# Optimization experiments

Hardware: AMD Instinct MI355X
Metric: run time of the kernel (lower is better)

The kernel has to match this reference:

```python
import jax, jax.numpy as jnp
import numpy as np

WINDOW = 10
STRIDES = 1
EPS = 1e-5


def setup_inputs() -> dict:
    key = jax.random.key(0)
    B, T, F = 128, 512, 40
    tensors = jax.random.normal(key, (B, T, F), dtype=jnp.float32)
    return {"tensors": tensors}


def reference(tensors):
    # tensors: [B, T, F]
    B, T, F = tensors.shape
    # window start positions, replicating the module's iter_list logic
    starts = np.arange(0, T - WINDOW + 1, STRIDES)
    if (T - WINDOW) not in starts:
        starts = np.append(starts, T - WINDOW)
    # [S, W] gather indices -> windowed view [B, S, W, F]
    idx = starts[:, None] + np.arange(WINDOW)[None, :]
    xw = tensors[:, idx, :]  # [B, S, W, F]

    mean = xw.mean(axis=2)  # [B, S, F] == K.mean over window axis
    # K.std: population std (ddof=0) over the window axis
    std = jnp.sqrt(((xw - mean[:, :, None, :]) ** 2).mean(axis=2))  # [B, S, F]
    # K.switch(is_nan(std), mean-mean, std): NaN std -> 0
    std = jnp.where(jnp.isnan(std), jnp.zeros_like(std), std) + EPS

    # E[x_i * x_j] over window for all feature pairs: [B, S, F, F]
    Exy = jnp.einsum('bswi,bswj->bsij', xw, xw) / WINDOW
    cov = Exy - mean[:, :, :, None] * mean[:, :, None, :]
    corr = cov / (std[:, :, :, None] * std[:, :, None, :])  # [B, S, F, F]

    # itertools.combinations(range(F), 2) order == upper-triangular row-major
    iu, ju = np.triu_indices(F, 1)
    return corr[:, :, iu, ju]  # [B, S, C] with C = F*(F-1)/2
```

## Files before the change

kernel.cpp:

```cpp
#include <hip/hip_runtime.h>

#define BB   128
#define TT   512
#define FF   40
#define WW   10
#define NS   503
#define NP   780
#define SC   64
#define NCHUNK 8
#define ROWS (SC + WW - 1)
#define EPSC 1e-5f
#define C01  0.31622776601683794f

__global__ __launch_bounds__(256, 4) void ts_corr_r6(const float* __restrict__ in,
                                                     float* __restrict__ out) {
    const int blk = blockIdx.x;
    const int b   = blk / NCHUNK;
    const int c   = blk - b * NCHUNK;
    const int s0  = (c == NCHUNK - 1) ? (NS - SC) : c * SC;
    const int tid = threadIdx.x;

    __shared__ float  xs[SC + WW][FF];
    __shared__ float2 st[SC][FF];

    const float4* src4 = (const float4*)(in + ((size_t)b * TT + s0) * FF);
    float4* xs4 = (float4*)&xs[0][0];
    #pragma unroll
    for (int k = 0; k < 3; ++k) {
        const int i = tid + k * 256;
        if (i < ROWS * FF / 4) xs4[i] = src4[i];
    }
    __syncthreads();

    #pragma unroll
    for (int k = 0; k < 3; ++k) {
        const int qd = tid + k * 256;
        if (qd < SC * FF / 4) {
            const int t  = qd / 10;
            const int f0 = (qd - t * 10) * 4;
            float sx0=0,sx1=0,sx2=0,sx3=0, sq0=0,sq1=0,sq2=0,sq3=0;
            #pragma unroll
            for (int w = 0; w < WW; ++w) {
                const float4 x = *(const float4*)&xs[t + w][f0];
                sx0 += x.x; sx1 += x.y; sx2 += x.z; sx3 += x.w;
                sq0 += x.x*x.x; sq1 += x.y*x.y; sq2 += x.z*x.z; sq3 += x.w*x.w;
            }
            const float m0 = sx0*0.1f, m1 = sx1*0.1f, m2 = sx2*0.1f, m3 = sx3*0.1f;
            const float u0 = 1.f/(sqrtf(fmaxf(sq0*0.1f - m0*m0, 0.f)) + EPSC);
            const float u1 = 1.f/(sqrtf(fmaxf(sq1*0.1f - m1*m1, 0.f)) + EPSC);
            const float u2 = 1.f/(sqrtf(fmaxf(sq2*0.1f - m2*m2, 0.f)) + EPSC);
            const float u3 = 1.f/(sqrtf(fmaxf(sq3*0.1f - m3*m3, 0.f)) + EPSC);
            *(float4*)&st[t][f0]     = make_float4(u0*C01, m0*u0, u1*C01, m1*u1);
            *(float4*)&st[t][f0 + 2] = make_float4(u2*C01, m2*u2, u3*C01, m3*u3);
        }
    }

    int pi[4], pj[4];
    float sxy[4], ph[4][WW];
    #pragma unroll
    for (int k = 0; k < 4; ++k) {
        const int p = tid + k * 256;
        const int pp = (p < NP) ? p : 0;
        int i = (int)((79.0f - sqrtf((float)(6241 - 8 * pp))) * 0.5f);
        while (i > 0 && i * (79 - i) / 2 > pp) --i;
        while ((i + 1) * (79 - (i + 1)) / 2 <= pp) ++i;
        pi[k] = i;
        pj[k] = pp - i * (79 - i) / 2 + i + 1;
        float s = 0.f;
        #pragma unroll
        for (int w = 0; w < WW; ++w) {
            const float pr = xs[w][pi[k]] * xs[w][pj[k]];
            ph[k][w] = pr;
            s += pr;
        }
        sxy[k] = s;
    }
    __syncthreads();

    float* dst0 = out + (size_t)(b * NS + s0) * NP + tid;

#define STEP2(U, TA, DO2) do {                                                  \
    const int _tA = (TA);                                                       \
    float* _dA = dst0 + (size_t)_tA * NP;                                       \
    float* _dB = _dA + NP;                                                      \
    _Pragma("unroll")                                                           \
    for (int k = 0; k < 3; ++k) {                                               \
        const int _ii = pi[k], _jj = pj[k];                                     \
        const float  _xiA = xs[_tA + WW][_ii], _xiB = xs[_tA + WW + 1][_ii];    \
        const float  _xjA = xs[_tA + WW][_jj], _xjB = xs[_tA + WW + 1][_jj];    \
        const float2 _siA = st[_tA][_ii],      _siB = st[_tA + 1][_ii];         \
        const float2 _sjA = st[_tA][_jj],      _sjB = st[_tA + 1][_jj];         \
        _dA[k * 256] = sxy[k] * _siA.x * _sjA.x - _siA.y * _sjA.y;              \
        const float _pn = _xiA * _xjA;                                          \
        sxy[k] += _pn - ph[k][U]; ph[k][U] = _pn;                               \
        _dB[k * 256] = sxy[k] * _siB.x * _sjB.x - _siB.y * _sjB.y;              \
        if (DO2) {                                                              \
            const float _p2 = _xiB * _xjB;                                      \
            sxy[k] += _p2 - ph[k][(U) + 1]; ph[k][(U) + 1] = _p2;               \
        }                                                                       \
    }                                                                           \
    if (tid < 12) {                                                             \
        const int _ii = pi[3], _jj = pj[3];                                     \
        const float  _xiA = xs[_tA + WW][_ii], _xiB = xs[_tA + WW + 1][_ii];    \
        const float  _xjA = xs[_tA + WW][_jj], _xjB = xs[_tA + WW + 1][_jj];    \
        const float2 _siA = st[_tA][_ii],      _siB = st[_tA + 1][_ii];         \
        const float2 _sjA = st[_tA][_jj],      _sjB = st[_tA + 1][_jj];         \
        _dA[768] = sxy[3] * _siA.x * _sjA.x - _siA.y * _sjA.y;                  \
        const float _pn = _xiA * _xjA;                                          \
        sxy[3] += _pn - ph[3][U]; ph[3][U] = _pn;                               \
        _dB[768] = sxy[3] * _siB.x * _sjB.x - _siB.y * _sjB.y;                  \
        if (DO2) {                                                              \
            const float _p2 = _xiB * _xjB;                                      \
            sxy[3] += _p2 - ph[3][(U) + 1]; ph[3][(U) + 1] = _p2;               \
        }                                                                       \
    }                                                                           \
} while (0)

    for (int t0 = 0; t0 < 60; t0 += WW) {
        STEP2(0, t0,     true);
        STEP2(2, t0 + 2, true);
        STEP2(4, t0 + 4, true);
        STEP2(6, t0 + 6, true);
        STEP2(8, t0 + 8, true);
    }
    STEP2(0, 60, true);
    STEP2(2, 62, false);
#undef STEP2
}

extern "C" void kernel_launch(void* const* d_in, const int* in_sizes, int n_in,
                              void* d_out, int out_size, void* d_ws, size_t ws_size,
                              hipStream_t stream) {
    const float* in = (const float*)d_in[0];
    float* out = (float*)d_out;
    ts_corr_r6<<<BB * NCHUNK, 256, 0, stream>>>(in, out);
}
```

Before: 47.34 us.

## Transpose shared tiles to feature-major, halve chunk size, slide stats incrementally

Stores the input tile and the per-time statistics transposed (feature-major with padded strides), so each pair thread reads consecutive time steps with float2/float4 shared loads. Halves the time chunk per block to 32, doubling the block count and raising the occupancy hint to 8. Window mean/std are computed with a running sliding sum over 8 consecutive steps instead of recomputing each window. More blocks mean the initial 10-step product sums and the overlapping input rows are recomputed more often relative to useful work, and the sliding variance may lose a little precision.

```diff
diff --git a/kernel.cpp b/kernel.cpp
--- a/kernel.cpp
+++ b/kernel.cpp
@@ -6,52 +6,62 @@
 #define WW   10
 #define NS   503
 #define NP   780
-#define SC   64
-#define NCHUNK 8
+#define SC   32
+#define NCHUNK 16
 #define ROWS (SC + WW - 1)
+#define XSTR 42
+#define SSTR 34
 #define EPSC 1e-5f
 #define C01  0.31622776601683794f
 
-__global__ __launch_bounds__(256, 4) void ts_corr_r6(const float* __restrict__ in,
+__global__ __launch_bounds__(256, 8) void ts_corr_r7(const float* __restrict__ in,
                                                      float* __restrict__ out) {
     const int blk = blockIdx.x;
-    const int b   = blk / NCHUNK;
-    const int c   = blk - b * NCHUNK;
+    const int b   = blk >> 4;
+    const int c   = blk & (NCHUNK - 1);
     const int s0  = (c == NCHUNK - 1) ? (NS - SC) : c * SC;
     const int tid = threadIdx.x;
 
-    __shared__ float  xs[SC + WW][FF];
-    __shared__ float2 st[SC][FF];
+    __shared__ __align__(16) float  xst[FF][XSTR];
+    __shared__ __align__(16) float2 stf[FF][SSTR];
 
     const float4* src4 = (const float4*)(in + ((size_t)b * TT + s0) * FF);
-    float4* xs4 = (float4*)&xs[0][0];
     #pragma unroll
-    for (int k = 0; k < 3; ++k) {
-        const int i = tid + k * 256;
-        if (i < ROWS * FF / 4) xs4[i] = src4[i];
+    for (int k = 0; k < 2; ++k) {
+        const int q = tid + k * 256;
+        if (q < ROWS * FF / 4) {
+            const int r  = q / 10;
+            const int f0 = (q - r * 10) * 4;
+            const float4 v = src4[q];
+            xst[f0    ][r] = v.x;
+            xst[f0 + 1][r] = v.y;
+            xst[f0 + 2][r] = v.z;
+            xst[f0 + 3][r] = v.w;
+        }
     }
     __syncthreads();
 
-    #pragma unroll
-    for (int k = 0; k < 3; ++k) {
-        const int qd = tid + k * 256;
-        if (qd < SC * FF / 4) {
-            const int t  = qd / 10;
-            const int f0 = (qd - t * 10) * 4;
-            float sx0=0,sx1=0,sx2=0,sx3=0, sq0=0,sq1=0,sq2=0,sq3=0;
-            #pragma unroll
-            for (int w = 0; w < WW; ++w) {
-                const float4 x = *(const float4*)&xs[t + w][f0];
-                sx0 += x.x; sx1 += x.y; sx2 += x.z; sx3 += x.w;
-                sq0 += x.x*x.x; sq1 += x.y*x.y; sq2 += x.z*x.z; sq3 += x.w*x.w;
+    if (tid < 160) {
+        const int f  = tid >> 2;
+        const int t0 = (tid & 3) * 8;
+        float sx = 0.f, sxx = 0.f;
+        #pragma unroll
+        for (int w = 0; w < WW; ++w) {
+            const float x = xst[f][t0 + w];
+            sx += x; sxx += x * x;
+        }
+        #pragma unroll
+        for (int u = 0; u < 8; ++u) {
+            const int t = t0 + u;
+            const float m  = sx * 0.1f;
+            const float vv = fmaxf(sxx * 0.1f - m * m, 0.f);
+            const float iu = 1.f / (sqrtf(vv) + EPSC);
+            stf[f][t] = make_float2(iu * C01, m * iu);
+            if (u < 7) {
+                const float xo = xst[f][t], xn = xst[f][t + WW];
+                sx  += xn - xo;
+                sxx += xn * xn - xo * xo;
             }
-            const float m0 = sx0*0.1f, m1 = sx1*0.1f, m2 = sx2*0.1f, m3 = sx3*0.1f;
-            const float u0 = 1.f/(sqrtf(fmaxf(sq0*0.1f - m0*m0, 0.f)) + EPSC);
-            const float u1 = 1.f/(sqrtf(fmaxf(sq1*0.1f - m1*m1, 0.f)) + EPSC);
-            const float u2 = 1.f/(sqrtf(fmaxf(sq2*0.1f - m2*m2, 0.f)) + EPSC);
-            const float u3 = 1.f/(sqrtf(fmaxf(sq3*0.1f - m3*m3, 0.f)) + EPSC);
-            *(float4*)&st[t][f0]     = make_float4(u0*C01, m0*u0, u1*C01, m1*u1);
-            *(float4*)&st[t][f0 + 2] = make_float4(u2*C01, m2*u2, u3*C01, m3*u3);
         }
     }
 
@@ -68,10 +78,13 @@
         pj[k] = pp - i * (79 - i) / 2 + i + 1;
         float s = 0.f;
         #pragma unroll
-        for (int w = 0; w < WW; ++w) {
-            const float pr = xs[w][pi[k]] * xs[w][pj[k]];
-            ph[k][w] = pr;
-            s += pr;
+        for (int w2 = 0; w2 < WW; w2 += 2) {
+            const float2 xi = *(const float2*)&xst[pi[k]][w2];
+            const float2 xj = *(const float2*)&xst[pj[k]][w2];
+            const float p0 = xi.x * xj.x, p1 = xi.y * xj.y;
+            ph[k][w2]     = p0;
+            ph[k][w2 + 1] = p1;
+            s += p0 + p1;
         }
         sxy[k] = s;
     }
@@ -85,46 +98,43 @@
     float* _dB = _dA + NP;                                                      \
     _Pragma("unroll")                                                           \
     for (int k = 0; k < 3; ++k) {                                               \
-        const int _ii = pi[k], _jj = pj[k];                                     \
-        const float  _xiA = xs[_tA + WW][_ii], _xiB = xs[_tA + WW + 1][_ii];    \
-        const float  _xjA = xs[_tA + WW][_jj], _xjB = xs[_tA + WW + 1][_jj];    \
-        const float2 _siA = st[_tA][_ii],      _siB = st[_tA + 1][_ii];         \
-        const float2 _sjA = st[_tA][_jj],      _sjB = st[_tA + 1][_jj];         \
-        _dA[k * 256] = sxy[k] * _siA.x * _sjA.x - _siA.y * _sjA.y;              \
-        const float _pn = _xiA * _xjA;                                          \
+        const float2 _xi = *(const float2*)&xst[pi[k]][_tA + WW];               \
+        const float2 _xj = *(const float2*)&xst[pj[k]][_tA + WW];               \
+        const float4 _si = *(const float4*)&stf[pi[k]][_tA];                    \
+        const float4 _sj = *(const float4*)&stf[pj[k]][_tA];                    \
+        _dA[k * 256] = sxy[k] * _si.x * _sj.x - _si.y * _sj.y;                  \
+        const float _pn = _xi.x * _xj.x;                                        \
         sxy[k] += _pn - ph[k][U]; ph[k][U] = _pn;                               \
-        _dB[k * 256] = sxy[k] * _siB.x * _sjB.x - _siB.y * _sjB.y;              \
+        _dB[k * 256] = sxy[k] * _si.z * _sj.z - _si.w * _sj.w;                  \
         if (DO2) {                                                              \
-            const float _p2 = _xiB * _xjB;                                      \
+            const float _p2 = _xi.y * _xj.y;                                    \
             sxy[k] += _p2 - ph[k][(U) + 1]; ph[k][(U) + 1] = _p2;               \
         }                                                                       \
     }                                                                           \
     if (tid < 12) {                                                             \
-        const int _ii = pi[3], _jj = pj[3];                                     \
-        const float  _xiA = xs[_tA + WW][_ii], _xiB = xs[_tA + WW + 1][_ii];    \
-        const float  _xjA = xs[_tA + WW][_jj], _xjB = xs[_tA + WW + 1][_jj];    \
-        const float2 _siA = st[_tA][_ii],      _siB = st[_tA + 1][_ii];         \
-        const float2 _sjA = st[_tA][_jj],      _sjB = st[_tA + 1][_jj];         \
-        _dA[768] = sxy[3] * _siA.x * _sjA.x - _siA.y * _sjA.y;                  \
-        const float _pn = _xiA * _xjA;                                          \
+        const float2 _xi = *(const float2*)&xst[pi[3]][_tA + WW];               \
+        const float2 _xj = *(const float2*)&xst[pj[3]][_tA + WW];               \
+        const float4 _si = *(const float4*)&stf[pi[3]][_tA];                    \
+        const float4 _sj = *(const float4*)&stf[pj[3]][_tA];                    \
+        _dA[768] = sxy[3] * _si.x * _sj.x - _si.y * _sj.y;                      \
+        const float _pn = _xi.x * _xj.x;                                        \
         sxy[3] += _pn - ph[3][U]; ph[3][U] = _pn;                               \
-        _dB[768] = sxy[3] * _siB.x * _sjB.x - _siB.y * _sjB.y;                  \
+        _dB[768] = sxy[3] * _si.z * _sj.z - _si.w * _sj.w;                      \
         if (DO2) {                                                              \
-            const float _p2 = _xiB * _xjB;                                      \
+            const float _p2 = _xi.y * _xj.y;                                    \
             sxy[3] += _p2 - ph[3][(U) + 1]; ph[3][(U) + 1] = _p2;               \
         }                                                                       \
     }                                                                           \
 } while (0)
 
-    for (int t0 = 0; t0 < 60; t0 += WW) {
+    for (int t0 = 0; t0 < 30; t0 += WW) {
         STEP2(0, t0,     true);
         STEP2(2, t0 + 2, true);
         STEP2(4, t0 + 4, true);
         STEP2(6, t0 + 6, true);
         STEP2(8, t0 + 8, true);
     }
-    STEP2(0, 60, true);
-    STEP2(2, 62, false);
+    STEP2(0, 30, false);
 #undef STEP2
 }
 
@@ -133,5 +143,5 @@
                               hipStream_t stream) {
     const float* in = (const float*)d_in[0];
     float* out = (float*)d_out;
-    ts_corr_r6<<<BB * NCHUNK, 256, 0, stream>>>(in, out);
+    ts_corr_r7<<<BB * NCHUNK, 256, 0, stream>>>(in, out);
 }
```

Measured after the change: 189.0 us. 299% more time.
